# Optimization experiments

Hardware: AMD Instinct MI355X
Metric: run time of the kernel (lower is better)

The kernel has to match this reference:

```python
import jax, jax.numpy as jnp
import numpy as np

N_HEAD = 16
D_HEAD = 64
D_MODEL = 1024  # d_qry = d_key = d_val
D_HIDDEN = N_HEAD * D_HEAD


def setup_inputs() -> dict:
    key = jax.random.key(0)
    ks = jax.random.split(key, 9)
    b, n = 2, 2048
    s = 0.02
    return {
        "qry": jax.random.normal(ks[0], (b, n, D_MODEL), jnp.float32),
        "key": jax.random.normal(ks[1], (b, n, D_MODEL), jnp.float32),
        "val": jax.random.normal(ks[2], (b, n, D_MODEL), jnp.float32),
        "mask": jax.random.randint(ks[3], (b, n), 0, 2) > 0,  # key-side padding mask
        "Wq": jax.random.normal(ks[4], (D_MODEL, D_HIDDEN), jnp.float32) * s,
        "Wk": jax.random.normal(ks[5], (D_MODEL, D_HIDDEN), jnp.float32) * s,
        "Wv": jax.random.normal(ks[6], (D_MODEL, D_HIDDEN), jnp.float32) * s,
        "Wo": jax.random.normal(ks[7], (D_HIDDEN, D_MODEL), jnp.float32) * s,
        "bo": jax.random.normal(ks[8], (D_MODEL,), jnp.float32) * s,
    }


def reference(qry, key, val, mask, Wq, Wk, Wv, Wo, bo):
    b, n, _ = qry.shape
    scale = D_HEAD ** 0.5
    # projections, split into heads: [b, h, n, d]
    q = (qry @ Wq).reshape(b, n, N_HEAD, D_HEAD).transpose(0, 2, 1, 3)
    k = (key @ Wk).reshape(b, n, N_HEAD, D_HEAD).transpose(0, 2, 1, 3)
    v = (val @ Wv).reshape(b, n, N_HEAD, D_HEAD).transpose(0, 2, 1, 3)
    sim = jnp.einsum('bhid,bhjd->bhij', q, k) / scale  # full O(n^2) scores
    # key-side padding mask broadcast over heads and query positions
    sim = jnp.where(mask[:, None, None, :], sim, jnp.float32(-1e32))
    attn = jax.nn.softmax(sim, axis=-1)
    # NOTE: original applies dropout to `sim` after computing attn (a no-op on
    # the output); dropout=0.0 regardless, so attention weights are `attn`.
    x = jnp.einsum('bhij,bhjd->bhid', attn, v)
    x = x.transpose(0, 2, 1, 3).reshape(b, n, D_HIDDEN)
    return x @ Wo + bo
```

## Files before the change

kernel.cpp:

```cpp
#include <hip/hip_runtime.h>
#include <hip/hip_bf16.h>

using u16 = unsigned short;
using u32 = unsigned int;
using short8 = __attribute__((ext_vector_type(8))) short;
using f32x4  = __attribute__((ext_vector_type(4))) float;
using u32x4  = __attribute__((ext_vector_type(4))) u32;
using u32x2  = __attribute__((ext_vector_type(2))) u32;

union V16 { u32x4 u; short8 s; };

__device__ __forceinline__ u16 f2b(float f) {
  u32 u = __float_as_uint(f);
  u32 r = (u + 0x7FFFu + ((u >> 16) & 1u)) >> 16;
  return (u16)r;
}
__device__ __forceinline__ u32 pk2(u16 a, u16 b) {
  return (u32)a | ((u32)b << 16);
}
__device__ __forceinline__ u32 cvtpk(float lo, float hi) {
  u32 r;
  asm("v_cvt_pk_bf16_f32 %0, %1, %2" : "=v"(r) : "v"(lo), "v"(hi));
  return r;
}
__device__ __forceinline__ float ex2(float x) {
  float r;
  asm("v_exp_f32 %0, %1" : "=v"(r) : "v"(x));
  return r;
}
__device__ __forceinline__ void gld16(const u16* g, u16* l) {
  __builtin_amdgcn_global_load_lds(
      (const __attribute__((address_space(1))) u32*)g,
      (__attribute__((address_space(3))) u32*)l, 16, 0, 0);
}

#define KSCALE 0.18033688011f
#define SMAX   12.0f


__global__ __launch_bounds__(256) void wconv(
    const float* __restrict__ Wq, const float* __restrict__ Wk,
    const float* __restrict__ Wv, const float* __restrict__ Wo,
    u16* __restrict__ Wt, u16* __restrict__ WoT)
{
  __shared__ u16 T[64][130];
  const int zz = blockIdx.z;
  const float* src = (zz == 0) ? Wq : (zz == 1) ? Wk : (zz == 2) ? Wv : Wo;
  u16* dst = (zz < 3) ? (Wt + (size_t)zz * 1048576) : WoT;
  const int nt = blockIdx.x, ks = blockIdx.y;
  const int tid = threadIdx.x;

  {
    const int kl = tid >> 2, nl0 = (tid & 3) * 32;
    const float* sp = src + (size_t)(ks * 64 + kl) * 1024 + nt * 128 + nl0;
#pragma unroll
    for (int i = 0; i < 8; ++i) {
      f32x4 x = *(const f32x4*)(sp + i * 4);
      T[kl][nl0 + i * 4 + 0] = f2b(x[0]);
      T[kl][nl0 + i * 4 + 1] = f2b(x[1]);
      T[kl][nl0 + i * 4 + 2] = f2b(x[2]);
      T[kl][nl0 + i * 4 + 3] = f2b(x[3]);
    }
  }
  __syncthreads();

  const int c = tid >> 4, l0 = (tid & 15) * 4;
  u16* dp = dst + ((size_t)(nt * 16 + ks) * 16 + c) * 512 + l0 * 8;
#pragma unroll
  for (int dl = 0; dl < 4; ++dl) {
    const int l = l0 + dl;
    const int kl = (c & 1) * 32 + (l >> 4) * 8;
    const int nl = (c >> 3) * 64 + ((c >> 1) & 3) * 16 + (l & 15);
    u32x4 u;
#pragma unroll
    for (int p = 0; p < 4; ++p)
      u[p] = pk2(T[kl + 2 * p][nl], T[kl + 2 * p + 1][nl]);
    *(u32x4*)(dp + dl * 8) = u;
  }
}

__global__ __launch_bounds__(256) void aconv(
    const float* __restrict__ Aq, const float* __restrict__ Ak,
    const float* __restrict__ Av, u16* __restrict__ Af,
    int z0, size_t zstride)
{
  const int z = blockIdx.z + z0;
  const float* A = (z == 0) ? Aq : (z == 1) ? Ak : Av;
  u16* dst = Af + (size_t)blockIdx.z * zstride;
  const int ks = blockIdx.x, mt = blockIdx.y;
  const int tid = threadIdx.x;
  const int r = tid >> 1, h = tid & 1;

  const f32x4* sp = (const f32x4*)(A + (size_t)(mt * 128 + r) * 1024 + ks * 64 + h * 32);
  const int c = ((r >> 6) << 3) | (((r >> 4) & 3) << 1) | h;
  u16* dp = dst + ((size_t)(mt * 16 + ks) * 16 + c) * 512 + (r & 15) * 8;

#pragma unroll
  for (int lg = 0; lg < 4; ++lg) {
    f32x4 x0 = sp[2 * lg], x1 = sp[2 * lg + 1];
    u32x4 u;
    u[0] = cvtpk(x0[0], x0[1]); u[1] = cvtpk(x0[2], x0[3]);
    u[2] = cvtpk(x1[0], x1[1]); u[3] = cvtpk(x1[2], x1[3]);
    *(u32x4*)(dp + lg * 128) = u;
  }
}

__global__ __launch_bounds__(256) void maskscan(
    const int* __restrict__ mask, int* __restrict__ cidx,
    float* __restrict__ cbias, int* __restrict__ ntb,
    u16* __restrict__ Kimg, u16* __restrict__ Vimg)
{
  const int h = blockIdx.x, b = blockIdx.y;
  const int tid = threadIdx.x;
  __shared__ int ssum[256];

  int m8[8], s = 0;
#pragma unroll
  for (int i = 0; i < 8; ++i) {
    m8[i] = mask[b * 2048 + tid * 8 + i] ? 1 : 0;
    s += m8[i];
  }
  ssum[tid] = s;
  __syncthreads();
  for (int off = 1; off < 256; off <<= 1) {
    int v = (tid >= off) ? ssum[tid - off] : 0;
    __syncthreads();
    ssum[tid] += v;
    __syncthreads();
  }
  const int nvalid = ssum[255];
  int run = ssum[tid] - s;

  if (h == 0) {
#pragma unroll
    for (int i = 0; i < 8; ++i) {
      cidx[b * 2048 + tid * 8 + i] = m8[i] ? run : -1;
      run += m8[i];
    }
#pragma unroll
    for (int i = 0; i < 8; ++i) {
      const int idx = tid * 8 + i;
      cbias[b * 2048 + idx] = (idx < nvalid) ? -SMAX : -1e30f;
    }
    if (tid == 0) ntb[b] = (nvalid + 63) >> 6;
  }

  const int pend = ((nvalid + 63) >> 6) << 6;
  for (int p = nvalid + tid; p < pend; p += 256) {
    const int kt2 = p >> 6, r = p & 63;
    const size_t base = ((size_t)((b * 16 + h) * 32 + kt2)) * 4096;
    const int t2 = ((r >> 5) << 1) | ((r >> 2) & 1);
    const int ll2 = (((r >> 3) & 3) << 2) | (r & 3);
#pragma unroll
    for (int s2 = 0; s2 < 2; ++s2)
#pragma unroll
      for (int lgk = 0; lgk < 4; ++lgk)
#pragma unroll
        for (int e = 0; e < 8; ++e)
          Kimg[base + (t2 * 2 + s2) * 512 + (lgk * 16 + ll2) * 8 + e] = 0;
    const int sv = r >> 5, lgv = (r >> 3) & 3, e0 = r & 7;
#pragma unroll
    for (int td = 0; td < 4; ++td)
#pragma unroll
      for (int llv = 0; llv < 16; ++llv)
        Vimg[base + (sv * 4 + td) * 512 + (lgv * 16 + llv) * 8 + e0] = 0;
  }
}

__global__ __launch_bounds__(512, 4) void gemm_qkv_k(
    const u16* __restrict__ Af, const u16* __restrict__ Wt,
    u16* __restrict__ Qw, u16* __restrict__ Kw, u16* __restrict__ Vw,
    const int* __restrict__ cidx, int z0, size_t azs)
{
  __shared__ u16 As[2][8192];
  __shared__ u16 Bs[2][8192];

  const int z = blockIdx.z + z0;
  const u16* Aimg = Af + (size_t)blockIdx.z * azs;
  const u16* Bimg = Wt + (size_t)z * 1048576;
  u16* O = (z == 0) ? Qw : (z == 1) ? Kw : Vw;

  const int tid = threadIdx.x;
  const int w = tid >> 6, l = tid & 63, lg = l >> 4, ll = l & 15;
  const int wr = w >> 2, wc = w & 3;
  const int nt = blockIdx.x, mt = blockIdx.y;
  const size_t ab = (size_t)mt * 131072;
  const size_t bb = (size_t)nt * 131072;

  f32x4 acc[4][2];
#pragma unroll
  for (int i = 0; i < 4; ++i)
#pragma unroll
    for (int t = 0; t < 2; ++t)
      acc[i][t] = (f32x4){0.f, 0.f, 0.f, 0.f};

#define QKV_ISSUE(ksx, buf) do {                                           \
    const size_t ao_ = ab + (size_t)(ksx) * 8192;                          \
    const size_t bo_ = bb + (size_t)(ksx) * 8192;                          \
    gld16(Aimg + ao_ + (size_t)w * 512 + l * 8,       &As[buf][w * 512]);  \
    gld16(Aimg + ao_ + (size_t)(w + 8) * 512 + l * 8, &As[buf][(w + 8) * 512]); \
    gld16(Bimg + bo_ + (size_t)w * 512 + l * 8,       &Bs[buf][w * 512]);  \
    gld16(Bimg + bo_ + (size_t)(w + 8) * 512 + l * 8, &Bs[buf][(w + 8) * 512]); \
  } while (0)

  QKV_ISSUE(0, 0);
  QKV_ISSUE(1, 1);

  for (int ks = 0; ks < 16; ++ks) {
    const int cur = ks & 1;
    if (ks < 15) asm volatile("s_waitcnt vmcnt(4)" ::: "memory");
    else         asm volatile("s_waitcnt vmcnt(0)" ::: "memory");
    __builtin_amdgcn_sched_barrier(0);
    __builtin_amdgcn_s_barrier();
    __builtin_amdgcn_sched_barrier(0);

    short8 afr[2][4], bfr[2][2];
#pragma unroll
    for (int kk = 0; kk < 2; ++kk) {
#pragma unroll
      for (int i = 0; i < 4; ++i) {
        V16 v; v.u = *(const u32x4*)&As[cur][(wr * 8 + i * 2 + kk) * 512 + l * 8];
        afr[kk][i] = v.s;
      }
#pragma unroll
      for (int t = 0; t < 2; ++t) {
        V16 v; v.u = *(const u32x4*)&Bs[cur][((wc >> 1) * 8 + ((wc & 1) * 2 + t) * 2 + kk) * 512 + l * 8];
        bfr[kk][t] = v.s;
      }
    }
#pragma unroll
    for (int kk = 0; kk < 2; ++kk)
#pragma unroll
      for (int i = 0; i < 4; ++i)
#pragma unroll
        for (int t = 0; t < 2; ++t)
          acc[i][t] = __builtin_amdgcn_mfma_f32_16x16x32_bf16(afr[kk][i], bfr[kk][t], acc[i][t], 0, 0, 0);

    asm volatile("s_waitcnt lgkmcnt(0)" ::: "memory");
    __builtin_amdgcn_sched_barrier(0);
    __builtin_amdgcn_s_barrier();
    __builtin_amdgcn_sched_barrier(0);
    if (ks + 2 < 16) QKV_ISSUE(ks + 2, cur);
  }
#undef QKV_ISSUE

  const int m0 = mt * 128, n0 = nt * 128;
  if (z == 0) {
#pragma unroll
    for (int i = 0; i < 4; ++i)
#pragma unroll
      for (int t = 0; t < 2; ++t) {
        const int n = n0 + wc * 32 + t * 16 + ll;
        const int h = n >> 6, dd = n & 63;
#pragma unroll
        for (int j = 0; j < 4; ++j) {
          const int m = m0 + wr * 64 + i * 16 + lg * 4 + j;
          const int bbk = m >> 11, pos = m & 2047;
          O[((size_t)(bbk * 16 + h) * 2048 + pos) * 64 + dd] = f2b(acc[i][t][j]);
        }
      }
  } else if (z == 1) {
#pragma unroll
    for (int i = 0; i < 4; ++i)
#pragma unroll
      for (int t = 0; t < 2; ++t) {
        const int n = n0 + wc * 32 + t * 16 + ll;
        const int h = n >> 6, dd = n & 63;
        const int s = dd >> 5, lgk = (dd >> 3) & 3, e = dd & 7;
        const int m_ = m0 + wr * 64 + i * 16 + lg * 4;
        const int bbk = m_ >> 11, pos0 = m_ & 2047;
        const int4 cp = *(const int4*)&cidx[bbk * 2048 + pos0];
        const int cpa[4] = {cp.x, cp.y, cp.z, cp.w};
#pragma unroll
        for (int j = 0; j < 4; ++j) {
          const int pp = cpa[j];
          if (pp >= 0) {
            const int kt2 = pp >> 6, r = pp & 63;
            const int t2 = ((r >> 5) << 1) | ((r >> 2) & 1);
            const int ll2 = (((r >> 3) & 3) << 2) | (r & 3);
            O[((size_t)((bbk * 16 + h) * 32 + kt2)) * 4096 + (t2 * 2 + s) * 512 + (lgk * 16 + ll2) * 8 + e]
                = f2b(acc[i][t][j] * KSCALE);
          }
        }
      }
  } else {
#pragma unroll
    for (int i = 0; i < 4; ++i)
#pragma unroll
      for (int t = 0; t < 2; ++t) {
        const int n = n0 + wc * 32 + t * 16 + ll;
        const int h = n >> 6, dd = n & 63;
        const int td = dd >> 4, llv = dd & 15;
        const int m_ = m0 + wr * 64 + i * 16 + lg * 4;
        const int bbk = m_ >> 11, pos0 = m_ & 2047;
        const int4 cp = *(const int4*)&cidx[bbk * 2048 + pos0];
        const int cpa[4] = {cp.x, cp.y, cp.z, cp.w};
#pragma unroll
        for (int j = 0; j < 4; ++j) {
          const int pp = cpa[j];
          if (pp >= 0) {
            const int kt2 = pp >> 6, kk = pp & 63;
            const int s = kk >> 5, lgv = (kk >> 3) & 3, e0 = kk & 7;
            O[((size_t)((bbk * 16 + h) * 32 + kt2)) * 4096 + (s * 4 + td) * 512 + (lgv * 16 + llv) * 8 + e0]
                = f2b(acc[i][t][j]);
          }
        }
      }
  }
}

__global__ __launch_bounds__(256) void attn_k(
    const u16* __restrict__ Q, const u16* __restrict__ Kt, const u16* __restrict__ Vt,
    const float* __restrict__ cbias, const int* __restrict__ ntb,
    u16* __restrict__ Xf)
{
  __shared__ u16 Ls[2][8192];

  const int tid = threadIdx.x;
  const int w = tid >> 6, l = tid & 63, lg = l >> 4, ll = l & 15;
  const int qb = blockIdx.x, h = blockIdx.y, b = blockIdx.z;
  const size_t qbase = (size_t)(b * 16 + h) * 2048 * 64;
  const size_t tbase = (size_t)((b * 16 + h) * 32) * 4096;
  const int q0 = qb * 128 + w * 32;
  const int ntiles = ntb[b];

  short8 aq[2][2];
#pragma unroll
  for (int g = 0; g < 2; ++g)
#pragma unroll
    for (int s = 0; s < 2; ++s) {
      V16 v; v.u = *(const u32x4*)&Q[qbase + (size_t)(q0 + g * 16 + ll) * 64 + s * 32 + lg * 8];
      aq[g][s] = v.s;
    }

  float lrow[2] = {0.f, 0.f};
  f32x4 o[2][4];
#pragma unroll
  for (int g = 0; g < 2; ++g)
#pragma unroll
    for (int td = 0; td < 4; ++td) o[g][td] = (f32x4){0.f, 0.f, 0.f, 0.f};

  u32x4 rg[4];
#pragma unroll
  for (int q = 0; q < 4; ++q) {
    const int c = w * 4 + q;
    const u16* src = (c < 8) ? Kt : Vt;
    rg[q] = *(const u32x4*)&src[tbase + (c & 7) * 512 + l * 8];
  }
#pragma unroll
  for (int q = 0; q < 4; ++q)
    *(u32x4*)&Ls[0][(w * 4 + q) * 512 + l * 8] = rg[q];
  if (ntiles > 1) {
#pragma unroll
    for (int q = 0; q < 4; ++q) {
      const int c = w * 4 + q;
      const u16* src = (c < 8) ? Kt : Vt;
      rg[q] = *(const u32x4*)&src[tbase + 4096 + (c & 7) * 512 + l * 8];
    }
  }
  asm volatile("s_waitcnt lgkmcnt(0)" ::: "memory");
  __builtin_amdgcn_sched_barrier(0);
  __builtin_amdgcn_s_barrier();
  __builtin_amdgcn_sched_barrier(0);

  for (int kt = 0; kt < ntiles; ++kt) {
    const int cur = kt & 1;
    const int j0 = kt * 64;
    const u16* Lc = Ls[cur];

    f32x4 sc[2][4];
    __builtin_amdgcn_s_setprio(1);
#pragma unroll
    for (int t = 0; t < 4; ++t) {
      short8 bk0, bk1;
      { V16 v; v.u = *(const u32x4*)&Lc[(t * 2 + 0) * 512 + l * 8]; bk0 = v.s; }
      { V16 v; v.u = *(const u32x4*)&Lc[(t * 2 + 1) * 512 + l * 8]; bk1 = v.s; }
      f32x4 a0 = (f32x4){0.f, 0.f, 0.f, 0.f};
      f32x4 a1 = (f32x4){0.f, 0.f, 0.f, 0.f};
      a0 = __builtin_amdgcn_mfma_f32_16x16x32_bf16(bk0, aq[0][0], a0, 0, 0, 0);
      a1 = __builtin_amdgcn_mfma_f32_16x16x32_bf16(bk0, aq[1][0], a1, 0, 0, 0);
      a0 = __builtin_amdgcn_mfma_f32_16x16x32_bf16(bk1, aq[0][1], a0, 0, 0, 0);
      a1 = __builtin_amdgcn_mfma_f32_16x16x32_bf16(bk1, aq[1][1], a1, 0, 0, 0);
      const f32x4 cb = *(const f32x4*)&cbias[b * 2048 + j0 + ((t >> 1) << 5) + ((t & 1) << 2) + (lg << 3)];
#pragma unroll
      for (int j = 0; j < 4; ++j) {
        sc[0][t][j] = a0[j] + cb[j];
        sc[1][t][j] = a1[j] + cb[j];
      }
    }
    __builtin_amdgcn_s_setprio(0);

#pragma unroll
    for (int g = 0; g < 2; ++g) {
      f32x4 s4 = (f32x4){0.f, 0.f, 0.f, 0.f};
#pragma unroll
      for (int t = 0; t < 4; ++t)
#pragma unroll
        for (int j = 0; j < 4; ++j) {
          sc[g][t][j] = ex2(sc[g][t][j]);
          s4[j] += sc[g][t][j];
        }
      float rs = (s4[0] + s4[1]) + (s4[2] + s4[3]);
      rs += __shfl_xor(rs, 16);
      rs += __shfl_xor(rs, 32);
      lrow[g] += rs;
    }

    __builtin_amdgcn_s_setprio(1);
#pragma unroll
    for (int s = 0; s < 2; ++s) {
      V16 pb0, pb1;
      pb0.u[0] = cvtpk(sc[0][2 * s][0], sc[0][2 * s][1]);
      pb0.u[1] = cvtpk(sc[0][2 * s][2], sc[0][2 * s][3]);
      pb0.u[2] = cvtpk(sc[0][2 * s + 1][0], sc[0][2 * s + 1][1]);
      pb0.u[3] = cvtpk(sc[0][2 * s + 1][2], sc[0][2 * s + 1][3]);
      pb1.u[0] = cvtpk(sc[1][2 * s][0], sc[1][2 * s][1]);
      pb1.u[1] = cvtpk(sc[1][2 * s][2], sc[1][2 * s][3]);
      pb1.u[2] = cvtpk(sc[1][2 * s + 1][0], sc[1][2 * s + 1][1]);
      pb1.u[3] = cvtpk(sc[1][2 * s + 1][2], sc[1][2 * s + 1][3]);
#pragma unroll
      for (int td = 0; td < 4; ++td) {
        V16 v; v.u = *(const u32x4*)&Lc[4096 + (s * 4 + td) * 512 + l * 8];
        o[0][td] = __builtin_amdgcn_mfma_f32_16x16x32_bf16(v.s, pb0.s, o[0][td], 0, 0, 0);
        o[1][td] = __builtin_amdgcn_mfma_f32_16x16x32_bf16(v.s, pb1.s, o[1][td], 0, 0, 0);
      }
    }
    __builtin_amdgcn_s_setprio(0);

    if (kt + 1 < ntiles) {
#pragma unroll
      for (int q = 0; q < 4; ++q)
        *(u32x4*)&Ls[cur ^ 1][(w * 4 + q) * 512 + l * 8] = rg[q];
    }
    if (kt + 2 < ntiles) {
#pragma unroll
      for (int q = 0; q < 4; ++q) {
        const int c = w * 4 + q;
        const u16* src = (c < 8) ? Kt : Vt;
        rg[q] = *(const u32x4*)&src[tbase + (size_t)(kt + 2) * 4096 + (c & 7) * 512 + l * 8];
      }
    }
    asm volatile("s_waitcnt lgkmcnt(0)" ::: "memory");
    __builtin_amdgcn_sched_barrier(0);
    __builtin_amdgcn_s_barrier();
    __builtin_amdgcn_sched_barrier(0);
  }

#pragma unroll
  for (int g = 0; g < 2; ++g) {
    const float inv = 1.f / lrow[g];
    const int m = b * 2048 + q0 + g * 16 + ll;
    const int mt = m >> 7, mr = m & 127;
    const int e0 = (lg & 1) * 4;
#pragma unroll
    for (int td = 0; td < 4; ++td) {
      const int c = ((mr >> 6) << 3) | (((mr >> 4) & 3) << 1) | (td >> 1);
      const int lA = (((td << 1) + (lg >> 1)) & 3) * 16 + (mr & 15);
      u32x2 wv;
      wv[0] = cvtpk(o[g][td][0] * inv, o[g][td][1] * inv);
      wv[1] = cvtpk(o[g][td][2] * inv, o[g][td][3] * inv);
      *(u32x2*)&Xf[((size_t)(mt * 16 + h) * 16 + c) * 512 + lA * 8 + e0] = wv;
    }
  }
}

__global__ __launch_bounds__(512, 4) void gemm_out_k(
    const u16* __restrict__ Xf, const u16* __restrict__ WoF,
    const float* __restrict__ bo, float* __restrict__ out)
{
  __shared__ u16 As[2][8192];
  __shared__ u16 Bs[2][8192];

  const int tid = threadIdx.x;
  const int w = tid >> 6, l = tid & 63, lg = l >> 4, ll = l & 15;
  const int wr = w >> 2, wc = w & 3;
  const int nt = blockIdx.x, mt = blockIdx.y;
  const size_t ab = (size_t)mt * 131072;
  const size_t bb = (size_t)nt * 131072;

  f32x4 acc[4][2];
#pragma unroll
  for (int i = 0; i < 4; ++i)
#pragma unroll
    for (int t = 0; t < 2; ++t)
      acc[i][t] = (f32x4){0.f, 0.f, 0.f, 0.f};

#define OUT_ISSUE(ksx, buf) do {                                           \
    const size_t ao_ = ab + (size_t)(ksx) * 8192;                          \
    const size_t bo_ = bb + (size_t)(ksx) * 8192;                          \
    gld16(Xf + ao_ + (size_t)w * 512 + l * 8,        &As[buf][w * 512]);   \
    gld16(Xf + ao_ + (size_t)(w + 8) * 512 + l * 8,  &As[buf][(w + 8) * 512]); \
    gld16(WoF + bo_ + (size_t)w * 512 + l * 8,       &Bs[buf][w * 512]);   \
    gld16(WoF + bo_ + (size_t)(w + 8) * 512 + l * 8, &Bs[buf][(w + 8) * 512]); \
  } while (0)

  OUT_ISSUE(0, 0);
  OUT_ISSUE(1, 1);

  for (int ks = 0; ks < 16; ++ks) {
    const int cur = ks & 1;
    if (ks < 15) asm volatile("s_waitcnt vmcnt(4)" ::: "memory");
    else         asm volatile("s_waitcnt vmcnt(0)" ::: "memory");
    __builtin_amdgcn_sched_barrier(0);
    __builtin_amdgcn_s_barrier();
    __builtin_amdgcn_sched_barrier(0);

    short8 afr[2][4], bfr[2][2];
#pragma unroll
    for (int kk = 0; kk < 2; ++kk) {
#pragma unroll
      for (int i = 0; i < 4; ++i) {
        V16 v; v.u = *(const u32x4*)&As[cur][(wr * 8 + i * 2 + kk) * 512 + l * 8];
        afr[kk][i] = v.s;
      }
#pragma unroll
      for (int t = 0; t < 2; ++t) {
        V16 v; v.u = *(const u32x4*)&Bs[cur][((wc >> 1) * 8 + ((wc & 1) * 2 + t) * 2 + kk) * 512 + l * 8];
        bfr[kk][t] = v.s;
      }
    }
#pragma unroll
    for (int kk = 0; kk < 2; ++kk)
#pragma unroll
      for (int i = 0; i < 4; ++i)
#pragma unroll
        for (int t = 0; t < 2; ++t)
          acc[i][t] = __builtin_amdgcn_mfma_f32_16x16x32_bf16(afr[kk][i], bfr[kk][t], acc[i][t], 0, 0, 0);

    asm volatile("s_waitcnt lgkmcnt(0)" ::: "memory");
    __builtin_amdgcn_sched_barrier(0);
    __builtin_amdgcn_s_barrier();
    __builtin_amdgcn_sched_barrier(0);
    if (ks + 2 < 16) OUT_ISSUE(ks + 2, cur);
  }
#undef OUT_ISSUE

  const int m0 = mt * 128, n0 = nt * 128;
#pragma unroll
  for (int i = 0; i < 4; ++i)
#pragma unroll
    for (int t = 0; t < 2; ++t) {
      const int n = n0 + wc * 32 + t * 16 + ll;
      const float bv = bo[n];
#pragma unroll
      for (int j = 0; j < 4; ++j) {
        const int m = m0 + wr * 64 + i * 16 + lg * 4 + j;
        out[(size_t)m * 1024 + n] = acc[i][t][j] + bv;
      }
    }
}

extern "C" void kernel_launch(void* const* d_in, const int* in_sizes, int n_in,
                              void* d_out, int out_size, void* d_ws, size_t ws_size,
                              hipStream_t stream) {
  const float* qry = (const float*)d_in[0];
  const float* key = (const float*)d_in[1];
  const float* val = (const float*)d_in[2];
  const int* mask  = (const int*)d_in[3];
  const float* Wq  = (const float*)d_in[4];
  const float* Wk  = (const float*)d_in[5];
  const float* Wv  = (const float*)d_in[6];
  const float* Wo  = (const float*)d_in[7];
  const float* bo  = (const float*)d_in[8];
  float* out = (float*)d_out;

  char* ws = (char*)d_ws;
  u16* Wt  = (u16*)(ws);
  u16* WoT = (u16*)(ws + 6291456);
  u16* Qw  = (u16*)(ws + 8388608);
  u16* Kw  = (u16*)(ws + 16777216);
  u16* Vw  = (u16*)(ws + 25165824);
  u16* Af  = (u16*)(ws + 33554432);
  u16* Xw  = (u16*)(ws + 33554432);

  int*   cidx  = (int*)d_out;
  float* cbias = (float*)((char*)d_out + 16384);
  int*   ntb   = (int*)((char*)d_out + 32768);

  wconv<<<dim3(8, 16, 4), 256, 0, stream>>>(Wq, Wk, Wv, Wo, Wt, WoT);
  maskscan<<<dim3(16, 2), 256, 0, stream>>>(mask, cidx, cbias, ntb, Kw, Vw);

  const bool big = (ws_size >= 58720256ull);
  if (big) {
    aconv<<<dim3(16, 32, 3), 256, 0, stream>>>(qry, key, val, Af, 0, 4194304);
    gemm_qkv_k<<<dim3(8, 32, 3), 512, 0, stream>>>(Af, Wt, Qw, Kw, Vw, cidx, 0, 4194304);
  } else {
    for (int z = 0; z < 3; ++z) {
      aconv<<<dim3(16, 32, 1), 256, 0, stream>>>(qry, key, val, Af, z, 0);
      gemm_qkv_k<<<dim3(8, 32, 1), 512, 0, stream>>>(Af, Wt, Qw, Kw, Vw, cidx, z, 0);
    }
  }
  attn_k<<<dim3(16, 16, 2), 256, 0, stream>>>(Qw, Kw, Vw, cbias, ntb, Xw);
  gemm_out_k<<<dim3(8, 32, 1), 512, 0, stream>>>(Xw, WoT, bo, out);
}
```

Baseline: 113.1 us.

## Triple-buffer GEMM LDS stages and remap blocks for XCD-local tile reuse

```diff
diff --git a/kernel.cpp b/kernel.cpp
--- a/kernel.cpp
+++ b/kernel.cpp
@@ -172,18 +172,23 @@
     u16* __restrict__ Qw, u16* __restrict__ Kw, u16* __restrict__ Vw,
     const int* __restrict__ cidx, int z0, size_t azs)
 {
-  __shared__ u16 As[2][8192];
-  __shared__ u16 Bs[2][8192];
-
-  const int z = blockIdx.z + z0;
-  const u16* Aimg = Af + (size_t)blockIdx.z * azs;
+  __shared__ u16 As[3][8192];
+  __shared__ u16 Bs[3][8192];
+
+  const int L = blockIdx.x;
+  const int xcd = L & 7, idx = L >> 3;
+  const int mt = (xcd << 2) | (idx & 3);
+  const int nt = (idx >> 2) & 7;
+  const int zi = idx >> 5;
+  const int z = z0 + zi;
+
+  const u16* Aimg = Af + (size_t)zi * azs;
   const u16* Bimg = Wt + (size_t)z * 1048576;
   u16* O = (z == 0) ? Qw : (z == 1) ? Kw : Vw;
 
   const int tid = threadIdx.x;
   const int w = tid >> 6, l = tid & 63, lg = l >> 4, ll = l & 15;
   const int wr = w >> 2, wc = w & 3;
-  const int nt = blockIdx.x, mt = blockIdx.y;
   const size_t ab = (size_t)mt * 131072;
   const size_t bb = (size_t)nt * 131072;
 
@@ -207,13 +212,15 @@
   QKV_ISSUE(1, 1);
 
   for (int ks = 0; ks < 16; ++ks) {
-    const int cur = ks & 1;
+    const int cur = ks % 3;
     if (ks < 15) asm volatile("s_waitcnt vmcnt(4)" ::: "memory");
     else         asm volatile("s_waitcnt vmcnt(0)" ::: "memory");
     __builtin_amdgcn_sched_barrier(0);
     __builtin_amdgcn_s_barrier();
     __builtin_amdgcn_sched_barrier(0);
 
+    if (ks + 2 < 16) QKV_ISSUE(ks + 2, (ks + 2) % 3);
+
     short8 afr[2][4], bfr[2][2];
 #pragma unroll
     for (int kk = 0; kk < 2; ++kk) {
@@ -235,12 +242,6 @@
 #pragma unroll
         for (int t = 0; t < 2; ++t)
           acc[i][t] = __builtin_amdgcn_mfma_f32_16x16x32_bf16(afr[kk][i], bfr[kk][t], acc[i][t], 0, 0, 0);
-
-    asm volatile("s_waitcnt lgkmcnt(0)" ::: "memory");
-    __builtin_amdgcn_sched_barrier(0);
-    __builtin_amdgcn_s_barrier();
-    __builtin_amdgcn_sched_barrier(0);
-    if (ks + 2 < 16) QKV_ISSUE(ks + 2, cur);
   }
 #undef QKV_ISSUE
 
@@ -468,13 +469,17 @@
     const u16* __restrict__ Xf, const u16* __restrict__ WoF,
     const float* __restrict__ bo, float* __restrict__ out)
 {
-  __shared__ u16 As[2][8192];
-  __shared__ u16 Bs[2][8192];
+  __shared__ u16 As[3][8192];
+  __shared__ u16 Bs[3][8192];
+
+  const int L = blockIdx.x;
+  const int xcd = L & 7, idx = L >> 3;
+  const int mt = (xcd << 2) | (idx & 3);
+  const int nt = idx >> 2;
 
   const int tid = threadIdx.x;
   const int w = tid >> 6, l = tid & 63, lg = l >> 4, ll = l & 15;
   const int wr = w >> 2, wc = w & 3;
-  const int nt = blockIdx.x, mt = blockIdx.y;
   const size_t ab = (size_t)mt * 131072;
   const size_t bb = (size_t)nt * 131072;
 
@@ -498,13 +503,15 @@
   OUT_ISSUE(1, 1);
 
   for (int ks = 0; ks < 16; ++ks) {
-    const int cur = ks & 1;
+    const int cur = ks % 3;
     if (ks < 15) asm volatile("s_waitcnt vmcnt(4)" ::: "memory");
     else         asm volatile("s_waitcnt vmcnt(0)" ::: "memory");
     __builtin_amdgcn_sched_barrier(0);
     __builtin_amdgcn_s_barrier();
     __builtin_amdgcn_sched_barrier(0);
 
+    if (ks + 2 < 16) OUT_ISSUE(ks + 2, (ks + 2) % 3);
+
     short8 afr[2][4], bfr[2][2];
 #pragma unroll
     for (int kk = 0; kk < 2; ++kk) {
@@ -526,12 +533,6 @@
 #pragma unroll
         for (int t = 0; t < 2; ++t)
           acc[i][t] = __builtin_amdgcn_mfma_f32_16x16x32_bf16(afr[kk][i], bfr[kk][t], acc[i][t], 0, 0, 0);
-
-    asm volatile("s_waitcnt lgkmcnt(0)" ::: "memory");
-    __builtin_amdgcn_sched_barrier(0);
-    __builtin_amdgcn_s_barrier();
-    __builtin_amdgcn_sched_barrier(0);
-    if (ks + 2 < 16) OUT_ISSUE(ks + 2, cur);
   }
 #undef OUT_ISSUE
 
@@ -583,13 +584,13 @@
   const bool big = (ws_size >= 58720256ull);
   if (big) {
     aconv<<<dim3(16, 32, 3), 256, 0, stream>>>(qry, key, val, Af, 0, 4194304);
-    gemm_qkv_k<<<dim3(8, 32, 3), 512, 0, stream>>>(Af, Wt, Qw, Kw, Vw, cidx, 0, 4194304);
+    gemm_qkv_k<<<dim3(768, 1, 1), 512, 0, stream>>>(Af, Wt, Qw, Kw, Vw, cidx, 0, 4194304);
   } else {
     for (int z = 0; z < 3; ++z) {
       aconv<<<dim3(16, 32, 1), 256, 0, stream>>>(qry, key, val, Af, z, 0);
-      gemm_qkv_k<<<dim3(8, 32, 1), 512, 0, stream>>>(Af, Wt, Qw, Kw, Vw, cidx, z, 0);
+      gemm_qkv_k<<<dim3(256, 1, 1), 512, 0, stream>>>(Af, Wt, Qw, Kw, Vw, cidx, z, 0);
     }
   }
   attn_k<<<dim3(16, 16, 2), 256, 0, stream>>>(Qw, Kw, Vw, cbias, ntb, Xw);
-  gemm_out_k<<<dim3(8, 32, 1), 512, 0, stream>>>(Xw, WoT, bo, out);
-}
+  gemm_out_k<<<dim3(256, 1, 1), 512, 0, stream>>>(Xw, WoT, bo, out);
+}
```

Measured after the change: 107.0 us. 5.4% less time.
